# Kernel optimization log

Measured on AMD Instinct MI355X. Metric: run time of the kernel, lower is better.

The kernel has to match this reference:

```python
import jax, jax.numpy as jnp
import numpy as np

FEAT_STRIDE = 8
IM_DIMS = (4096.0, 4096.0)  # (height, width)
ANCHOR_SCALES = (8.0, 16.0, 32.0)
RATIOS = (0.5, 1.0, 2.0)
PRE_NMS_TOPN = 12000   # TRAIN cfg (eval_mode=False)
POST_NMS_TOPN = 2000
NMS_THRESH = 0.7
MIN_SIZE = 16.0


def _generate_anchors(base_size=16.0, ratios=RATIOS, scales=ANCHOR_SCALES):
    ratios = np.array(ratios, np.float32)
    scales = np.array(scales, np.float32)
    w = h = float(base_size)
    x_ctr = 0.5 * (w - 1.0)
    y_ctr = 0.5 * (h - 1.0)
    size = w * h
    ws = np.round(np.sqrt(size / ratios))
    hs = np.round(ws * ratios)
    out = []
    for wr, hr in zip(ws, hs):
        wss = wr * scales
        hss = hr * scales
        out.append(np.stack([x_ctr - 0.5 * (wss - 1.0), y_ctr - 0.5 * (hss - 1.0),
                             x_ctr + 0.5 * (wss - 1.0), y_ctr + 0.5 * (hss - 1.0)], axis=1))
    return np.concatenate(out, 0).astype(np.float32)  # [A=9, 4]


def _nms(boxes, scores, thresh, max_out):
    # greedy sequential NMS; indices are discrete -> stop gradients here
    boxes = jax.lax.stop_gradient(boxes)
    scores = jax.lax.stop_gradient(scores)
    areas = (boxes[:, 2] - boxes[:, 0] + 1.0) * (boxes[:, 3] - boxes[:, 1] + 1.0)

    def body(i, state):
        supp, keep = state
        idx = jnp.argmax(jnp.where(supp, -jnp.inf, scores))
        b = boxes[idx]
        xx1 = jnp.maximum(b[0], boxes[:, 0])
        yy1 = jnp.maximum(b[1], boxes[:, 1])
        xx2 = jnp.minimum(b[2], boxes[:, 2])
        yy2 = jnp.minimum(b[3], boxes[:, 3])
        inter = jnp.maximum(0.0, xx2 - xx1 + 1.0) * jnp.maximum(0.0, yy2 - yy1 + 1.0)
        iou = inter / (areas[idx] + areas - inter)
        supp = supp | (iou > thresh)  # also suppresses idx itself (iou==1)
        keep = keep.at[i].set(idx.astype(jnp.int32))
        return supp, keep

    supp0 = jnp.zeros(boxes.shape[0], dtype=bool)
    keep0 = jnp.zeros(max_out, dtype=jnp.int32)
    _, keep = jax.lax.fori_loop(0, max_out, body, (supp0, keep0))
    return keep


def reference(rpn_cls_score, rpn_bbox_pred):
    _, H, W, C2 = rpn_cls_score.shape
    A = C2 // 2
    # rpn_softmax: per-anchor 2-way (bg, fg) softmax; channels laid out [2, A]
    prob = jax.nn.softmax(rpn_cls_score.reshape(H, W, 2, A), axis=2)
    scores = prob[:, :, 1, :].reshape(-1)           # fg scores, [H*W*A]
    deltas = rpn_bbox_pred.reshape(-1, 4)           # [H*W*A, 4]

    # anchors shifted over the feature grid
    anchors = jnp.asarray(_generate_anchors())       # [A, 4]
    sx = jnp.arange(W, dtype=jnp.float32) * FEAT_STRIDE
    sy = jnp.arange(H, dtype=jnp.float32) * FEAT_STRIDE
    shift_x, shift_y = jnp.meshgrid(sx, sy)          # [H, W]
    shifts = jnp.stack([shift_x, shift_y, shift_x, shift_y], -1).reshape(-1, 1, 4)
    all_anchors = (anchors[None, :, :] + shifts).reshape(-1, 4)  # [H*W*A, 4]

    # bbox_transform_inv
    ws = all_anchors[:, 2] - all_anchors[:, 0] + 1.0
    hs = all_anchors[:, 3] - all_anchors[:, 1] + 1.0
    cx = all_anchors[:, 0] + 0.5 * ws
    cy = all_anchors[:, 1] + 0.5 * hs
    dx, dy, dw, dh = deltas[:, 0], deltas[:, 1], deltas[:, 2], deltas[:, 3]
    pcx = dx * ws + cx
    pcy = dy * hs + cy
    pw = jnp.exp(dw) * ws
    ph = jnp.exp(dh) * hs
    x1 = pcx - 0.5 * pw
    y1 = pcy - 0.5 * ph
    x2 = pcx + 0.5 * pw
    y2 = pcy + 0.5 * ph

    # clip to image boundaries
    x1 = jnp.clip(x1, 0.0, IM_DIMS[1] - 1.0)
    y1 = jnp.clip(y1, 0.0, IM_DIMS[0] - 1.0)
    x2 = jnp.clip(x2, 0.0, IM_DIMS[1] - 1.0)
    y2 = jnp.clip(y2, 0.0, IM_DIMS[0] - 1.0)
    proposals = jnp.stack([x1, y1, x2, y2], axis=1)

    # drop tiny boxes (jit-friendly: -inf score instead of physical removal)
    keep_min = ((x2 - x1 + 1.0) >= MIN_SIZE) & ((y2 - y1 + 1.0) >= MIN_SIZE)
    scores = jnp.where(keep_min, scores, -jnp.inf)

    top_scores, order = jax.lax.top_k(scores, PRE_NMS_TOPN)
    props = proposals[order]                         # [pre_nms_topN, 4]
    keep = _nms(props, top_scores, NMS_THRESH, POST_NMS_TOPN)
    rois = props[keep]                               # [post_nms_topN, 4]
    # blob: [batch_idx(=0), x1, y1, x2, y2]
    return jnp.concatenate([jnp.zeros((POST_NMS_TOPN, 1), rois.dtype), rois], axis=1)


def setup_inputs() -> dict:
    key = jax.random.key(0)
    k1, k2 = jax.random.split(key)
    rpn_cls_score = jax.random.normal(k1, (1, 512, 512, 18), dtype=jnp.float32)
    rpn_bbox_pred = jax.random.normal(k2, (1, 512, 512, 36), dtype=jnp.float32) * 0.2
    return {"rpn_cls_score": rpn_cls_score, "rpn_bbox_pred": rpn_bbox_pred}
```

## Files before the change

kernel.cpp:

```cpp
#include <hip/hip_runtime.h>
#include <cstdint>
#include <cstddef>

#pragma clang fp contract(off)

#define N_ANCH 2359296
#define K_PRE  12000
#define K_POST 2000
#define NWORD  188
#define NC     94
#define TIE_CAP 65536

typedef unsigned int u32;
typedef unsigned long long u64;

__constant__ float c_anch[9][4] = {
  { -84.f,  -40.f,   99.f,   55.f },
  { -176.f, -88.f,  191.f,  103.f },
  { -360.f, -184.f, 375.f,  199.f },
  { -56.f,  -56.f,   71.f,   71.f },
  { -120.f, -120.f, 135.f,  135.f },
  { -248.f, -248.f, 263.f,  263.f },
  { -36.f,  -80.f,   51.f,   95.f },
  { -80.f,  -168.f,  95.f,  183.f },
  { -168.f, -344.f, 183.f,  359.f },
};

__device__ __forceinline__ float pexpf(float xin) {
#pragma clang fp contract(off)
  const float exp_hi = 88.3762626647950f;
  const float exp_lo = -88.3762626647949f;
  const float LOG2EF = 1.44269504088896341f;
  const float C1 = 0.693359375f;
  const float C2 = -2.12194440e-4f;
  const float p0 = 1.9875691500E-4f;
  const float p1 = 1.3981999507E-3f;
  const float p2 = 8.3334519073E-3f;
  const float p3 = 4.1665795894E-2f;
  const float p4 = 1.6666665459E-1f;
  const float p5 = 5.0000001201E-1f;
  float x = fminf(fmaxf(xin, exp_lo), exp_hi);
  float fx = floorf(x * LOG2EF + 0.5f);
  float tmp = C1 * fx;
  float z = C2 * fx;
  x = x - tmp;
  x = x - z;
  z = x * x;
  float y = x * p0 + p1;
  y = y * x + p2;
  y = y * x + p3;
  y = y * x + p4;
  y = y * x + p5;
  y = y * z + x;
  y = 1.0f + y;
  int n = (int)fx;
  u32 e = ((u32)(n + 127)) << 23;
  return y * __uint_as_float(e);
}

__device__ __forceinline__ void decode_box(const float* __restrict__ bbox, int aidx,
                                           float4* ob, float* oarea, bool* okeep) {
#pragma clang fp contract(off)
  int pos = aidx / 9;
  int a = aidx - pos * 9;
  int w = pos & 511;
  int h = pos >> 9;
  float shx = (float)(w * 8);
  float shy = (float)(h * 8);
  float ax1 = c_anch[a][0] + shx;
  float ay1 = c_anch[a][1] + shy;
  float ax2 = c_anch[a][2] + shx;
  float ay2 = c_anch[a][3] + shy;
  float aw = (ax2 - ax1) + 1.0f;
  float ah = (ay2 - ay1) + 1.0f;
  float acx = ax1 + 0.5f * aw;
  float acy = ay1 + 0.5f * ah;
  const float* d = bbox + (size_t)pos * 36 + (size_t)a * 4;
  float dx = d[0], dy = d[1], dw = d[2], dh = d[3];
  float pcx = dx * aw + acx;
  float pcy = dy * ah + acy;
  float pw = pexpf(dw) * aw;
  float ph = pexpf(dh) * ah;
  float x1 = pcx - 0.5f * pw;
  float y1 = pcy - 0.5f * ph;
  float x2 = pcx + 0.5f * pw;
  float y2 = pcy + 0.5f * ph;
  x1 = fminf(fmaxf(x1, 0.0f), 4095.0f);
  y1 = fminf(fmaxf(y1, 0.0f), 4095.0f);
  x2 = fminf(fmaxf(x2, 0.0f), 4095.0f);
  y2 = fminf(fmaxf(y2, 0.0f), 4095.0f);
  *ob = make_float4(x1, y1, x2, y2);
  float ww = (x2 - x1) + 1.0f;
  float hh = (y2 - y1) + 1.0f;
  *oarea = ww * hh;
  *okeep = (ww >= 16.0f) && (hh >= 16.0f);
}

__global__ void k_scores(const float* __restrict__ cls, const float* __restrict__ bbox,
                         u32* __restrict__ keys, u32* __restrict__ ctl,
                         u32* __restrict__ hist) {
#pragma clang fp contract(off)
  int t = blockIdx.x * blockDim.x + threadIdx.x;
  if (blockIdx.x == 0) {
    if (threadIdx.x < 16) ctl[threadIdx.x] = (threadIdx.x == 1) ? (u32)K_PRE : 0u;
    if (threadIdx.x < 256) hist[threadIdx.x] = 0u;
  }
  if (t >= N_ANCH) return;
  int pos = t / 9;
  int a = t - pos * 9;
  float s0 = cls[(size_t)pos * 18 + a];
  float s1 = cls[(size_t)pos * 18 + 9 + a];
  float m = fmaxf(s0, s1);
  float e0 = pexpf(s0 - m);
  float e1 = pexpf(s1 - m);
  float p = e1 / (e0 + e1);
  float4 box; float area; bool km;
  decode_box(bbox, t, &box, &area, &km);
  keys[t] = km ? (__float_as_uint(p) | 0x80000000u) : 0u;
}

__global__ void __launch_bounds__(1024) k_histscan(const u32* __restrict__ keys,
                                                   u32* __restrict__ ctl,
                                                   u32* __restrict__ hist,
                                                   int shift, int pass) {
  __shared__ u32 lh[4][256];
  __shared__ u32 s_last;
  int t = threadIdx.x;
  if (t < 256) { lh[0][t] = 0u; lh[1][t] = 0u; lh[2][t] = 0u; lh[3][t] = 0u; }
  __syncthreads();
  int sub = t & 3;
  u32 prefix = ctl[0];
  u32 msk = (shift == 24) ? 0u : (0xFFFFFFFFu << (shift + 8));
  int stride = gridDim.x * blockDim.x;
  for (int i = blockIdx.x * blockDim.x + t; i < N_ANCH; i += stride) {
    u32 k = keys[i];
    if ((k & msk) == prefix) atomicAdd(&lh[sub][(k >> shift) & 0xFFu], 1u);
  }
  __syncthreads();
  if (t < 256) {
    u32 hsum = lh[0][t] + lh[1][t] + lh[2][t] + lh[3][t];
    if (hsum) atomicAdd(&hist[t], hsum);
  }
  __syncthreads();
  if (t == 0) {
    __threadfence();
    u32 old = atomicAdd(&ctl[8 + pass], 1u);
    s_last = (old == gridDim.x - 1) ? 1u : 0u;
  }
  __syncthreads();
  if (!s_last) return;
  __threadfence();
  __shared__ u32 sh[256];
  __shared__ u32 horig[256];
  __shared__ int s_d;
  u32 h = 0;
  if (t < 256) {
    h = atomicAdd(&hist[t], 0u);
    sh[t] = h; horig[t] = h;
  }
  if (t == 0) s_d = 0;
  u32 krem = ctl[1];
  __syncthreads();
  u32 v = h;
  for (int off = 1; off < 256; off <<= 1) {
    u32 add = (t < 256 && t + off < 256) ? sh[t + off] : 0u;
    __syncthreads();
    if (t < 256) { v += add; sh[t] = v; }
    __syncthreads();
  }
  if (t < 256 && sh[t] >= krem) atomicMax(&s_d, t);
  __syncthreads();
  if (t == 0) {
    int d = s_d;
    u32 cum = sh[d] - horig[d];
    ctl[0] |= ((u32)d) << shift;
    ctl[1] = krem - cum;
    if (shift == 0) { ctl[2] = ctl[0]; ctl[3] = ctl[1]; }
  }
  if (t < 256) hist[t] = 0u;
}

__global__ void __launch_bounds__(1024) k_collect(const u32* __restrict__ keys,
                                                  u32* __restrict__ ctl,
                                                  int* __restrict__ sel,
                                                  int* __restrict__ tie,
                                                  u64* __restrict__ comps) {
  __shared__ int stI[2048];
  __shared__ u64 stC[2048];
  __shared__ int stT[256];
  __shared__ u32 s_cnt, s_tcnt, s_base, s_tbase;
  int tid = threadIdx.x;
  if (tid == 0) { s_cnt = 0; s_tcnt = 0; }
  __syncthreads();
  u32 kstar = ctl[2];
  int stride = gridDim.x * blockDim.x;
  for (int i = blockIdx.x * blockDim.x + tid; i < N_ANCH; i += stride) {
    u32 k = keys[i];
    if (k > kstar) {
      u32 p = atomicAdd(&s_cnt, 1u);
      u64 cmp = ((u64)k << 32) | (u64)(0xFFFFFFFFu - (u32)i);
      if (p < 2048u) { stI[p] = i; stC[p] = cmp; }
      else { u32 g = atomicAdd(&ctl[4], 1u); sel[g] = i; comps[g] = cmp; }
    } else if (k == kstar) {
      u32 p = atomicAdd(&s_tcnt, 1u);
      if (p < 256u) stT[p] = i;
      else { u32 g = atomicAdd(&ctl[5], 1u); if (g < TIE_CAP) tie[g] = i; }
    }
  }
  __syncthreads();
  if (tid == 0) {
    u32 n = min(s_cnt, 2048u);
    s_base = atomicAdd(&ctl[4], n);
    u32 tn = min(s_tcnt, 256u);
    s_tbase = atomicAdd(&ctl[5], tn);
  }
  __syncthreads();
  u32 n = min(s_cnt, 2048u);
  for (u32 q = tid; q < n; q += blockDim.x) {
    sel[s_base + q] = stI[q];
    comps[s_base + q] = stC[q];
  }
  u32 tn = min(s_tcnt, 256u);
  for (u32 q = tid; q < tn; q += blockDim.x) {
    u32 g = s_tbase + q;
    if (g < TIE_CAP) tie[g] = stT[q];
  }
}

__global__ void k_tiepick(const u32* __restrict__ ctl, const int* __restrict__ tie,
                          int* __restrict__ sel, u64* __restrict__ comps) {
  u32 T = ctl[5]; if (T > TIE_CAP) T = TIE_CAP;
  if (T > 8192u) T = 8192u;
  u32 need = ctl[3];
  u32 base = ctl[4];
  u32 kstar = ctl[2];
  for (u32 t = threadIdx.x; t < T; t += blockDim.x) {
    int v = tie[t];
    u32 r = 0;
    for (u32 u = 0; u < T; ++u) r += (tie[u] < v) ? 1u : 0u;
    if (r < need) {
      sel[base + r] = v;
      comps[base + r] = ((u64)kstar << 32) | (u64)(0xFFFFFFFFu - (u32)v);
    }
  }
}

__global__ void k_rankdec(const u64* __restrict__ comps, const int* __restrict__ sel,
                          const float* __restrict__ bbox,
                          float4* __restrict__ props, float* __restrict__ areas) {
  __shared__ u64 tile[2048];
  int tid = threadIdx.x;
  int lane = tid & 63;
  int wave = tid >> 6;
  int base = (blockIdx.x * 4 + wave) * 8;
  u64 c0 = comps[base + 0], c1 = comps[base + 1], c2 = comps[base + 2], c3 = comps[base + 3];
  u64 c4 = comps[base + 4], c5 = comps[base + 5], c6 = comps[base + 6], c7 = comps[base + 7];
  int n0 = 0, n1 = 0, n2 = 0, n3 = 0, n4 = 0, n5 = 0, n6 = 0, n7 = 0;
  for (int t0 = 0; t0 < K_PRE; t0 += 2048) {
    int cnt = min(2048, K_PRE - t0);
    __syncthreads();
    for (int q = tid; q < cnt; q += 256) tile[q] = comps[t0 + q];
    __syncthreads();
    for (int q = lane; q < cnt; q += 64) {
      u64 v = tile[q];
      n0 += (v > c0); n1 += (v > c1); n2 += (v > c2); n3 += (v > c3);
      n4 += (v > c4); n5 += (v > c5); n6 += (v > c6); n7 += (v > c7);
    }
  }
  for (int off = 32; off; off >>= 1) {
    n0 += __shfl_xor(n0, off); n1 += __shfl_xor(n1, off);
    n2 += __shfl_xor(n2, off); n3 += __shfl_xor(n3, off);
    n4 += __shfl_xor(n4, off); n5 += __shfl_xor(n5, off);
    n6 += __shfl_xor(n6, off); n7 += __shfl_xor(n7, off);
  }
  int rk = n0;
  rk = (lane == 1) ? n1 : rk; rk = (lane == 2) ? n2 : rk;
  rk = (lane == 3) ? n3 : rk; rk = (lane == 4) ? n4 : rk;
  rk = (lane == 5) ? n5 : rk; rk = (lane == 6) ? n6 : rk;
  rk = (lane == 7) ? n7 : rk;
  if (lane < 8) {
    float4 box; float area; bool km;
    decode_box(bbox, sel[base + lane], &box, &area, &km);
    props[rk] = box;
    areas[rk] = area;
  }
}

__device__ __forceinline__ int d2idx(int c, int h, int lane) {
  return ((c * 2 + h) * 64 + lane) * 2;
}

__global__ void k_mask(const float4* __restrict__ props, const float* __restrict__ areas,
                       u64* __restrict__ mask, u64* __restrict__ diag2,
                       u64* __restrict__ sub2) {
#pragma clang fp contract(off)
  int x = blockIdx.x, y = blockIdx.y;
  int cx = x >> 1, cy = y >> 1;
  if (cy + 1 < cx || cy == cx + 1) return;
  __shared__ float4 bj[64];
  __shared__ float aj[64];
  int j0 = y * 64;
  bj[threadIdx.x] = props[j0 + threadIdx.x];
  aj[threadIdx.x] = areas[j0 + threadIdx.x];
  __syncthreads();
  int i = x * 64 + threadIdx.x;
  float4 bi = props[i];
  float ai = areas[i];
  u64 bits = 0;
  for (int jj = 0; jj < 64; ++jj) {
    int j = j0 + jj;
    float4 bb = bj[jj];
    float xx1 = fmaxf(bi.x, bb.x);
    float yy1 = fmaxf(bi.y, bb.y);
    float xx2 = fminf(bi.z, bb.z);
    float yy2 = fminf(bi.w, bb.w);
    float w = fmaxf(0.0f, (xx2 - xx1) + 1.0f);
    float h = fmaxf(0.0f, (yy2 - yy1) + 1.0f);
    float inter = w * h;
    float iou = inter / ((ai + aj[jj]) - inter);
    if ((iou > 0.7f) && (j < K_PRE)) bits |= (1ull << jj);
  }
  if (cy == cx)          diag2[d2idx(cx, x & 1, threadIdx.x) + (y & 1)] = bits;
  else if (cy == cx - 1) sub2[d2idx(cx, x & 1, threadIdx.x) + (y & 1)] = bits;
  else                   mask[(size_t)i * NWORD + y] = bits;
}

#define NMS_BAR() asm volatile("s_waitcnt lgkmcnt(0)\n\ts_barrier" ::: "memory")

typedef __attribute__((address_space(1))) const u32* gas_p;
typedef __attribute__((address_space(3))) u32* las_p;
__device__ __forceinline__ void gll16(const u64* g, u64* l) {
  __builtin_amdgcn_global_load_lds((gas_p)g, (las_p)l, 16, 0, 0);
}

__global__ void __launch_bounds__(1024, 1) k_nms(const u64* __restrict__ mask,
                                                 const u64* __restrict__ diag2,
                                                 const u64* __restrict__ sub2,
                                                 const float4* __restrict__ props,
                                                 float* __restrict__ out) {
  __shared__ u64 rem[NWORD];
  __shared__ int keepb[K_POST];
  __shared__ int kept[2][128];
  __shared__ u64 dstage[2][2][64][2];
  __shared__ u64 sstage[2][2][64][2];
  __shared__ int s_kk[2];
  __shared__ int s_nk;
  __shared__ int s_brk;
  int tid = threadIdx.x;
  int lane = tid & 63;
  int wave = tid >> 6;
  for (int w = tid; w < NWORD; w += 1024) {
    int base = w * 64;
    u64 v;
    if (base + 64 <= K_PRE) v = 0ull;
    else if (base >= K_PRE) v = ~0ull;
    else v = (~0ull) << (K_PRE - base);
    rem[w] = v;
  }
  if (tid == 0) { s_nk = 0; s_brk = 0; s_kk[0] = 0; s_kk[1] = 0; }
  if (wave == 0) {
    gll16(diag2 + d2idx(0, 0, lane), &dstage[0][0][0][0]);
    gll16(diag2 + d2idx(0, 1, lane), &dstage[0][1][0][0]);
    gll16(sub2 + d2idx(1, 0, lane), &sstage[1][0][0][0]);
    gll16(sub2 + d2idx(1, 1, lane), &sstage[1][1][0][0]);
  }
  __syncthreads();

  int nk = 0;

  for (int c = 0; c < NC; ++c) {
    if (s_brk) break;
    int par = c & 1;
    if (wave == 0) {
      int cn = min(c + 1, NC - 1);
      int cs = min(c + 2, NC - 1);
      gll16(diag2 + d2idx(cn, 0, lane), &dstage[cn & 1][0][0][0]);
      gll16(diag2 + d2idx(cn, 1, lane), &dstage[cn & 1][1][0][0]);
      gll16(sub2 + d2idx(cs, 0, lane), &sstage[cs & 1][0][0][0]);
      gll16(sub2 + d2idx(cs, 1, lane), &sstage[cs & 1][1][0][0]);
      asm volatile("s_waitcnt vmcnt(4)" ::: "memory");
      u64 dl0A = dstage[par][0][lane][0], dl1A = dstage[par][0][lane][1];
      u64 dh0A = dstage[par][1][lane][0], dh1A = dstage[par][1][lane][1];
      int ps = (c + 1) & 1;
      u64 sl0A = sstage[ps][0][lane][0], sl1A = sstage[ps][0][lane][1];
      u64 sh0A = sstage[ps][1][lane][0], sh1A = sstage[ps][1][lane][1];
      u64 w0 = ~rem[2 * c];
      u64 w1 = ~rem[2 * c + 1];
      u64 km0 = 0, km1 = 0;
      int nk0 = nk;
      while (w0 != 0ull && nk < K_POST) {
        int j = (int)__builtin_ctzll(w0);
        u64 sup = __ballot((int)((dl0A >> j) & 1ull));
        km0 |= (1ull << j);
        nk++;
        w0 &= ~sup;
      }
      if (km0) w1 &= ~__ballot((int)((dh0A & km0) != 0ull));
      while (w1 != 0ull && nk < K_POST) {
        int j = (int)__builtin_ctzll(w1);
        u64 sup = __ballot((int)((dh1A >> j) & 1ull));
        km1 |= (1ull << j);
        nk++;
        w1 &= ~sup;
      }
      int ncnt0 = __popcll(km0);
      u64 below = (1ull << lane) - 1ull;
      if ((km0 >> lane) & 1ull) {
        int pos = nk0 + __popcll(km0 & below);
        int idx = (c << 7) | lane;
        keepb[pos] = idx;
        kept[par][pos - nk0] = idx;
      }
      if ((km1 >> lane) & 1ull) {
        int pos = nk0 + ncnt0 + __popcll(km1 & below);
        int idx = (c << 7) | 64 | lane;
        keepb[pos] = idx;
        kept[par][pos - nk0] = idx;
      }
      if (c + 1 < NC) {
        int plo = (int)((((sl0A & km0) | (sl1A & km1)) != 0ull) ? 1 : 0);
        int phi = (int)((((sh0A & km0) | (sh1A & km1)) != 0ull) ? 1 : 0);
        u64 vlo = __ballot(plo);
        u64 vhi = __ballot(phi);
        if (lane == 0) {
          if (vlo) atomicOr((unsigned long long*)&rem[2 * c + 2], (unsigned long long)vlo);
          if (vhi) atomicOr((unsigned long long*)&rem[2 * c + 3], (unsigned long long)vhi);
        }
      }
      if (lane == 0) { s_kk[par] = nk - nk0; s_nk = nk; s_brk = (nk >= K_POST) ? 1 : 0; }
    } else if (c >= 1) {
      int kkp = s_kk[par ^ 1];
      const int* kb = &kept[par ^ 1][0];
      int wv = wave - 1;
      int seg = wv % 3;
      int q0 = wv / 3;
      int w = 2 * c + 2 + seg * 64 + lane;
      if (kkp > q0 && w < NWORD) {
        int m = kkp - 1;
        const u64* p0 = mask + (size_t)kb[q0] * NWORD + w;
        const u64* p1 = mask + (size_t)kb[min(q0 + 5, m)] * NWORD + w;
        const u64* p2 = mask + (size_t)kb[min(q0 + 10, m)] * NWORD + w;
        const u64* p3 = mask + (size_t)kb[min(q0 + 15, m)] * NWORD + w;
        const u64* p4 = mask + (size_t)kb[min(q0 + 20, m)] * NWORD + w;
        const u64* p5 = mask + (size_t)kb[min(q0 + 25, m)] * NWORD + w;
        const u64* p6 = mask + (size_t)kb[min(q0 + 30, m)] * NWORD + w;
        const u64* p7 = mask + (size_t)kb[min(q0 + 35, m)] * NWORD + w;
        u64 fp0, fp1, fp2, fp3, fp4, fp5, fp6, fp7;
        asm volatile(
          "global_load_dwordx2 %0, %8, off\n\t"
          "global_load_dwordx2 %1, %9, off\n\t"
          "global_load_dwordx2 %2, %10, off\n\t"
          "global_load_dwordx2 %3, %11, off\n\t"
          "global_load_dwordx2 %4, %12, off\n\t"
          "global_load_dwordx2 %5, %13, off\n\t"
          "global_load_dwordx2 %6, %14, off\n\t"
          "global_load_dwordx2 %7, %15, off\n\t"
          "s_waitcnt vmcnt(0)"
          : "=&v"(fp0), "=&v"(fp1), "=&v"(fp2), "=&v"(fp3),
            "=&v"(fp4), "=&v"(fp5), "=&v"(fp6), "=&v"(fp7)
          : "v"(p0), "v"(p1), "v"(p2), "v"(p3),
            "v"(p4), "v"(p5), "v"(p6), "v"(p7)
          : "memory");
        u64 v = (fp0 | fp1) | (fp2 | fp3) | ((fp4 | fp5) | (fp6 | fp7));
        for (int q = q0 + 40; q < kkp; q += 5)
          v |= mask[(size_t)kb[q] * NWORD + w];
        if (v) atomicOr((unsigned long long*)&rem[w], (unsigned long long)v);
      }
    }
    NMS_BAR();
  }
  __syncthreads();
  int fnk = s_nk;
  for (int t = tid; t < K_POST; t += 1024) {
    int kidx = (t < fnk) ? keepb[t] : 0;
    float4 b = props[kidx];
    out[t * 5 + 0] = 0.0f;
    out[t * 5 + 1] = b.x;
    out[t * 5 + 2] = b.y;
    out[t * 5 + 3] = b.z;
    out[t * 5 + 4] = b.w;
  }
}

extern "C" void kernel_launch(void* const* d_in, const int* in_sizes, int n_in,
                              void* d_out, int out_size, void* d_ws, size_t ws_size,
                              hipStream_t stream) {
  const float* cls  = (const float*)d_in[0];
  const float* bbox = (const float*)d_in[1];
  float* out = (float*)d_out;
  char* ws = (char*)d_ws;

  u64* mask    = (u64*)ws;
  u32* keys    = (u32*)ws;
  u32* ctl     = (u32*)(ws + 9437184);
  u32* hist    = (u32*)(ws + 9437248);
  int* sel     = (int*)(ws + 9438464);
  int* tie     = (int*)(ws + 9486592);
  u64* comps   = (u64*)(ws + 18096128);
  float4* props= (float4*)(ws + 18240512);
  float* areas = (float*)(ws + 18433024);
  u64* diag2   = (u64*)(ws + 18481152);
  u64* sub2    = (u64*)(ws + 18673664);

  k_scores<<<dim3((N_ANCH + 255) / 256), dim3(256), 0, stream>>>(cls, bbox, keys, ctl, hist);
  const int shifts[4] = {24, 16, 8, 0};
  for (int s = 0; s < 4; ++s)
    k_histscan<<<dim3(256), dim3(1024), 0, stream>>>(keys, ctl, hist, shifts[s], s);
  k_collect<<<dim3(256), dim3(1024), 0, stream>>>(keys, ctl, sel, tie, comps);
  k_tiepick<<<dim3(1), dim3(256), 0, stream>>>(ctl, tie, sel, comps);
  k_rankdec<<<dim3(375), dim3(256), 0, stream>>>(comps, sel, bbox, props, areas);
  k_mask<<<dim3(188, 188), dim3(64), 0, stream>>>(props, areas, mask, diag2, sub2);
  k_nms<<<dim3(1), dim3(1024), 0, stream>>>(mask, diag2, sub2, props, out);
}
```

Before: 304.8 us.

## Widen NMS chunks to 256 boxes to halve block barriers

```diff
diff --git a/kernel.cpp b/kernel.cpp
--- a/kernel.cpp
+++ b/kernel.cpp
@@ -8,7 +8,7 @@
 #define K_PRE  12000
 #define K_POST 2000
 #define NWORD  188
-#define NC     94
+#define NC     47
 #define TIE_CAP 65536
 
 typedef unsigned int u32;
@@ -286,17 +286,18 @@
   }
 }
 
-__device__ __forceinline__ int d2idx(int c, int h, int lane) {
-  return ((c * 2 + h) * 64 + lane) * 2;
+__device__ __forceinline__ size_t d4off(int c, int g, int h) {
+  return ((size_t)((c * 4 + g) * 2 + h)) * 128;
 }
 
 __global__ void k_mask(const float4* __restrict__ props, const float* __restrict__ areas,
-                       u64* __restrict__ mask, u64* __restrict__ diag2,
-                       u64* __restrict__ sub2) {
+                       u64* __restrict__ mask, u64* __restrict__ diag4,
+                       u64* __restrict__ sub4) {
 #pragma clang fp contract(off)
   int x = blockIdx.x, y = blockIdx.y;
-  int cx = x >> 1, cy = y >> 1;
-  if (cy + 1 < cx || cy == cx + 1) return;
+  int cx = x >> 2, cy = y >> 2;
+  bool wd = (cy == cx), ws = (cy == cx - 1), wf = (cy >= cx + 2);
+  if (!(wd || ws || wf)) return;
   __shared__ float4 bj[64];
   __shared__ float aj[64];
   int j0 = y * 64;
@@ -320,9 +321,16 @@
     float iou = inter / ((ai + aj[jj]) - inter);
     if ((iou > 0.7f) && (j < K_PRE)) bits |= (1ull << jj);
   }
-  if (cy == cx)          diag2[d2idx(cx, x & 1, threadIdx.x) + (y & 1)] = bits;
-  else if (cy == cx - 1) sub2[d2idx(cx, x & 1, threadIdx.x) + (y & 1)] = bits;
-  else                   mask[(size_t)i * NWORD + y] = bits;
+  int g = x & 3;
+  if (wd) {
+    int wi = y - 4 * cx;
+    diag4[d4off(cx, g, wi >> 1) + 2 * threadIdx.x + (wi & 1)] = bits;
+  } else if (ws) {
+    int wi = y - 4 * (cx - 1);
+    sub4[d4off(cx, g, wi >> 1) + 2 * threadIdx.x + (wi & 1)] = bits;
+  } else {
+    mask[(size_t)i * NWORD + y] = bits;
+  }
 }
 
 #define NMS_BAR() asm volatile("s_waitcnt lgkmcnt(0)\n\ts_barrier" ::: "memory")
@@ -334,15 +342,15 @@
 }
 
 __global__ void __launch_bounds__(1024, 1) k_nms(const u64* __restrict__ mask,
-                                                 const u64* __restrict__ diag2,
-                                                 const u64* __restrict__ sub2,
+                                                 const u64* __restrict__ diag4,
+                                                 const u64* __restrict__ sub4,
                                                  const float4* __restrict__ props,
                                                  float* __restrict__ out) {
   __shared__ u64 rem[NWORD];
   __shared__ int keepb[K_POST];
-  __shared__ int kept[2][128];
-  __shared__ u64 dstage[2][2][64][2];
-  __shared__ u64 sstage[2][2][64][2];
+  __shared__ int kept[2][256];
+  __shared__ u64 dstage[2][4][2][64][2];
+  __shared__ u64 sstage[2][4][2][64][2];
   __shared__ int s_kk[2];
   __shared__ int s_nk;
   __shared__ int s_brk;
@@ -359,10 +367,13 @@
   }
   if (tid == 0) { s_nk = 0; s_brk = 0; s_kk[0] = 0; s_kk[1] = 0; }
   if (wave == 0) {
-    gll16(diag2 + d2idx(0, 0, lane), &dstage[0][0][0][0]);
-    gll16(diag2 + d2idx(0, 1, lane), &dstage[0][1][0][0]);
-    gll16(sub2 + d2idx(1, 0, lane), &sstage[1][0][0][0]);
-    gll16(sub2 + d2idx(1, 1, lane), &sstage[1][1][0][0]);
+#pragma unroll
+    for (int g = 0; g < 4; ++g) {
+      gll16(diag4 + d4off(0, g, 0) + 2 * lane, &dstage[0][g][0][0][0]);
+      gll16(diag4 + d4off(0, g, 1) + 2 * lane, &dstage[0][g][1][0][0]);
+      gll16(sub4 + d4off(1, g, 0) + 2 * lane, &sstage[1][g][0][0][0]);
+      gll16(sub4 + d4off(1, g, 1) + 2 * lane, &sstage[1][g][1][0][0]);
+    }
   }
   __syncthreads();
 
@@ -374,57 +385,119 @@
     if (wave == 0) {
       int cn = min(c + 1, NC - 1);
       int cs = min(c + 2, NC - 1);
-      gll16(diag2 + d2idx(cn, 0, lane), &dstage[cn & 1][0][0][0]);
-      gll16(diag2 + d2idx(cn, 1, lane), &dstage[cn & 1][1][0][0]);
-      gll16(sub2 + d2idx(cs, 0, lane), &sstage[cs & 1][0][0][0]);
-      gll16(sub2 + d2idx(cs, 1, lane), &sstage[cs & 1][1][0][0]);
-      asm volatile("s_waitcnt vmcnt(4)" ::: "memory");
-      u64 dl0A = dstage[par][0][lane][0], dl1A = dstage[par][0][lane][1];
-      u64 dh0A = dstage[par][1][lane][0], dh1A = dstage[par][1][lane][1];
-      int ps = (c + 1) & 1;
-      u64 sl0A = sstage[ps][0][lane][0], sl1A = sstage[ps][0][lane][1];
-      u64 sh0A = sstage[ps][1][lane][0], sh1A = sstage[ps][1][lane][1];
-      u64 w0 = ~rem[2 * c];
-      u64 w1 = ~rem[2 * c + 1];
-      u64 km0 = 0, km1 = 0;
+#pragma unroll
+      for (int g = 0; g < 4; ++g) {
+        gll16(diag4 + d4off(cn, g, 0) + 2 * lane, &dstage[cn & 1][g][0][0][0]);
+        gll16(diag4 + d4off(cn, g, 1) + 2 * lane, &dstage[cn & 1][g][1][0][0]);
+        gll16(sub4 + d4off(cs, g, 0) + 2 * lane, &sstage[cs & 1][g][0][0][0]);
+        gll16(sub4 + d4off(cs, g, 1) + 2 * lane, &sstage[cs & 1][g][1][0][0]);
+      }
+      asm volatile("s_waitcnt vmcnt(16)" ::: "memory");
+      u64 w0 = ~rem[4 * c];
+      u64 w1 = ~rem[4 * c + 1];
+      u64 w2 = ~rem[4 * c + 2];
+      u64 w3 = ~rem[4 * c + 3];
+      u64 km0 = 0, km1 = 0, km2 = 0, km3 = 0;
       int nk0 = nk;
-      while (w0 != 0ull && nk < K_POST) {
-        int j = (int)__builtin_ctzll(w0);
-        u64 sup = __ballot((int)((dl0A >> j) & 1ull));
-        km0 |= (1ull << j);
-        nk++;
-        w0 &= ~sup;
-      }
-      if (km0) w1 &= ~__ballot((int)((dh0A & km0) != 0ull));
-      while (w1 != 0ull && nk < K_POST) {
-        int j = (int)__builtin_ctzll(w1);
-        u64 sup = __ballot((int)((dh1A >> j) & 1ull));
-        km1 |= (1ull << j);
-        nk++;
-        w1 &= ~sup;
-      }
-      int ncnt0 = __popcll(km0);
+      {
+        u64 d00 = dstage[par][0][0][lane][0];
+        while (w0 != 0ull && nk < K_POST) {
+          int j = (int)__builtin_ctzll(w0);
+          u64 sup = __ballot((int)((d00 >> j) & 1ull));
+          km0 |= (1ull << j);
+          nk++;
+          w0 &= ~sup;
+        }
+        if (km0) {
+          u64 d10 = dstage[par][1][0][lane][0];
+          u64 d20 = dstage[par][2][0][lane][0];
+          u64 d30 = dstage[par][3][0][lane][0];
+          w1 &= ~__ballot((int)((d10 & km0) != 0ull));
+          w2 &= ~__ballot((int)((d20 & km0) != 0ull));
+          w3 &= ~__ballot((int)((d30 & km0) != 0ull));
+        }
+      }
+      {
+        u64 d11 = dstage[par][1][0][lane][1];
+        while (w1 != 0ull && nk < K_POST) {
+          int j = (int)__builtin_ctzll(w1);
+          u64 sup = __ballot((int)((d11 >> j) & 1ull));
+          km1 |= (1ull << j);
+          nk++;
+          w1 &= ~sup;
+        }
+        if (km1) {
+          u64 d21 = dstage[par][2][0][lane][1];
+          u64 d31 = dstage[par][3][0][lane][1];
+          w2 &= ~__ballot((int)((d21 & km1) != 0ull));
+          w3 &= ~__ballot((int)((d31 & km1) != 0ull));
+        }
+      }
+      {
+        u64 d22 = dstage[par][2][1][lane][0];
+        while (w2 != 0ull && nk < K_POST) {
+          int j = (int)__builtin_ctzll(w2);
+          u64 sup = __ballot((int)((d22 >> j) & 1ull));
+          km2 |= (1ull << j);
+          nk++;
+          w2 &= ~sup;
+        }
+        if (km2) {
+          u64 d32 = dstage[par][3][1][lane][0];
+          w3 &= ~__ballot((int)((d32 & km2) != 0ull));
+        }
+      }
+      {
+        u64 d33 = dstage[par][3][1][lane][1];
+        while (w3 != 0ull && nk < K_POST) {
+          int j = (int)__builtin_ctzll(w3);
+          u64 sup = __ballot((int)((d33 >> j) & 1ull));
+          km3 |= (1ull << j);
+          nk++;
+          w3 &= ~sup;
+        }
+      }
+      int p0 = __popcll(km0), p1 = __popcll(km1), p2 = __popcll(km2);
       u64 below = (1ull << lane) - 1ull;
       if ((km0 >> lane) & 1ull) {
         int pos = nk0 + __popcll(km0 & below);
-        int idx = (c << 7) | lane;
-        keepb[pos] = idx;
-        kept[par][pos - nk0] = idx;
+        int idx = (c << 8) | lane;
+        keepb[pos] = idx; kept[par][pos - nk0] = idx;
       }
       if ((km1 >> lane) & 1ull) {
-        int pos = nk0 + ncnt0 + __popcll(km1 & below);
-        int idx = (c << 7) | 64 | lane;
-        keepb[pos] = idx;
-        kept[par][pos - nk0] = idx;
+        int pos = nk0 + p0 + __popcll(km1 & below);
+        int idx = (c << 8) | 64 | lane;
+        keepb[pos] = idx; kept[par][pos - nk0] = idx;
+      }
+      if ((km2 >> lane) & 1ull) {
+        int pos = nk0 + p0 + p1 + __popcll(km2 & below);
+        int idx = (c << 8) | 128 | lane;
+        keepb[pos] = idx; kept[par][pos - nk0] = idx;
+      }
+      if ((km3 >> lane) & 1ull) {
+        int pos = nk0 + p0 + p1 + p2 + __popcll(km3 & below);
+        int idx = (c << 8) | 192 | lane;
+        keepb[pos] = idx; kept[par][pos - nk0] = idx;
       }
       if (c + 1 < NC) {
-        int plo = (int)((((sl0A & km0) | (sl1A & km1)) != 0ull) ? 1 : 0);
-        int phi = (int)((((sh0A & km0) | (sh1A & km1)) != 0ull) ? 1 : 0);
-        u64 vlo = __ballot(plo);
-        u64 vhi = __ballot(phi);
+        int ps = (c + 1) & 1;
+        u64 a0 = (sstage[ps][0][0][lane][0] & km0) | (sstage[ps][0][0][lane][1] & km1)
+               | (sstage[ps][0][1][lane][0] & km2) | (sstage[ps][0][1][lane][1] & km3);
+        u64 a1 = (sstage[ps][1][0][lane][0] & km0) | (sstage[ps][1][0][lane][1] & km1)
+               | (sstage[ps][1][1][lane][0] & km2) | (sstage[ps][1][1][lane][1] & km3);
+        u64 a2 = (sstage[ps][2][0][lane][0] & km0) | (sstage[ps][2][0][lane][1] & km1)
+               | (sstage[ps][2][1][lane][0] & km2) | (sstage[ps][2][1][lane][1] & km3);
+        u64 a3 = (sstage[ps][3][0][lane][0] & km0) | (sstage[ps][3][0][lane][1] & km1)
+               | (sstage[ps][3][1][lane][0] & km2) | (sstage[ps][3][1][lane][1] & km3);
+        u64 v0 = __ballot((int)(a0 != 0ull));
+        u64 v1 = __ballot((int)(a1 != 0ull));
+        u64 v2 = __ballot((int)(a2 != 0ull));
+        u64 v3 = __ballot((int)(a3 != 0ull));
         if (lane == 0) {
-          if (vlo) atomicOr((unsigned long long*)&rem[2 * c + 2], (unsigned long long)vlo);
-          if (vhi) atomicOr((unsigned long long*)&rem[2 * c + 3], (unsigned long long)vhi);
+          if (v0) atomicOr((unsigned long long*)&rem[4 * c + 4], (unsigned long long)v0);
+          if (v1) atomicOr((unsigned long long*)&rem[4 * c + 5], (unsigned long long)v1);
+          if (v2) atomicOr((unsigned long long*)&rem[4 * c + 6], (unsigned long long)v2);
+          if (v3) atomicOr((unsigned long long*)&rem[4 * c + 7], (unsigned long long)v3);
         }
       }
       if (lane == 0) { s_kk[par] = nk - nk0; s_nk = nk; s_brk = (nk >= K_POST) ? 1 : 0; }
@@ -434,35 +507,39 @@
       int wv = wave - 1;
       int seg = wv % 3;
       int q0 = wv / 3;
-      int w = 2 * c + 2 + seg * 64 + lane;
+      int w = 4 * c + 4 + seg * 64 + lane;
       if (kkp > q0 && w < NWORD) {
         int m = kkp - 1;
-        const u64* p0 = mask + (size_t)kb[q0] * NWORD + w;
-        const u64* p1 = mask + (size_t)kb[min(q0 + 5, m)] * NWORD + w;
-        const u64* p2 = mask + (size_t)kb[min(q0 + 10, m)] * NWORD + w;
-        const u64* p3 = mask + (size_t)kb[min(q0 + 15, m)] * NWORD + w;
-        const u64* p4 = mask + (size_t)kb[min(q0 + 20, m)] * NWORD + w;
-        const u64* p5 = mask + (size_t)kb[min(q0 + 25, m)] * NWORD + w;
-        const u64* p6 = mask + (size_t)kb[min(q0 + 30, m)] * NWORD + w;
-        const u64* p7 = mask + (size_t)kb[min(q0 + 35, m)] * NWORD + w;
-        u64 fp0, fp1, fp2, fp3, fp4, fp5, fp6, fp7;
+        const u64* a0 = mask + (size_t)kb[q0] * NWORD + w;
+        const u64* a1 = mask + (size_t)kb[min(q0 + 5, m)] * NWORD + w;
+        const u64* a2 = mask + (size_t)kb[min(q0 + 10, m)] * NWORD + w;
+        const u64* a3 = mask + (size_t)kb[min(q0 + 15, m)] * NWORD + w;
+        const u64* a4 = mask + (size_t)kb[min(q0 + 20, m)] * NWORD + w;
+        const u64* a5 = mask + (size_t)kb[min(q0 + 25, m)] * NWORD + w;
+        const u64* a6 = mask + (size_t)kb[min(q0 + 30, m)] * NWORD + w;
+        const u64* a7 = mask + (size_t)kb[min(q0 + 35, m)] * NWORD + w;
+        const u64* a8 = mask + (size_t)kb[min(q0 + 40, m)] * NWORD + w;
+        const u64* a9 = mask + (size_t)kb[min(q0 + 45, m)] * NWORD + w;
+        u64 f0, f1, f2, f3, f4, f5, f6, f7, f8, f9;
         asm volatile(
-          "global_load_dwordx2 %0, %8, off\n\t"
-          "global_load_dwordx2 %1, %9, off\n\t"
-          "global_load_dwordx2 %2, %10, off\n\t"
-          "global_load_dwordx2 %3, %11, off\n\t"
-          "global_load_dwordx2 %4, %12, off\n\t"
-          "global_load_dwordx2 %5, %13, off\n\t"
-          "global_load_dwordx2 %6, %14, off\n\t"
-          "global_load_dwordx2 %7, %15, off\n\t"
+          "global_load_dwordx2 %0, %10, off\n\t"
+          "global_load_dwordx2 %1, %11, off\n\t"
+          "global_load_dwordx2 %2, %12, off\n\t"
+          "global_load_dwordx2 %3, %13, off\n\t"
+          "global_load_dwordx2 %4, %14, off\n\t"
+          "global_load_dwordx2 %5, %15, off\n\t"
+          "global_load_dwordx2 %6, %16, off\n\t"
+          "global_load_dwordx2 %7, %17, off\n\t"
+          "global_load_dwordx2 %8, %18, off\n\t"
+          "global_load_dwordx2 %9, %19, off\n\t"
           "s_waitcnt vmcnt(0)"
-          : "=&v"(fp0), "=&v"(fp1), "=&v"(fp2), "=&v"(fp3),
-            "=&v"(fp4), "=&v"(fp5), "=&v"(fp6), "=&v"(fp7)
-          : "v"(p0), "v"(p1), "v"(p2), "v"(p3),
-            "v"(p4), "v"(p5), "v"(p6), "v"(p7)
+          : "=&v"(f0), "=&v"(f1), "=&v"(f2), "=&v"(f3), "=&v"(f4),
+            "=&v"(f5), "=&v"(f6), "=&v"(f7), "=&v"(f8), "=&v"(f9)
+          : "v"(a0), "v"(a1), "v"(a2), "v"(a3), "v"(a4),
+            "v"(a5), "v"(a6), "v"(a7), "v"(a8), "v"(a9)
           : "memory");
-        u64 v = (fp0 | fp1) | (fp2 | fp3) | ((fp4 | fp5) | (fp6 | fp7));
-        for (int q = q0 + 40; q < kkp; q += 5)
+        u64 v = ((f0 | f1) | (f2 | f3)) | ((f4 | f5) | (f6 | f7)) | (f8 | f9);
+        for (int q = q0 + 50; q < kkp; q += 5)
           v |= mask[(size_t)kb[q] * NWORD + w];
         if (v) atomicOr((unsigned long long*)&rem[w], (unsigned long long)v);
       }
@@ -499,8 +576,8 @@
   u64* comps   = (u64*)(ws + 18096128);
   float4* props= (float4*)(ws + 18240512);
   float* areas = (float*)(ws + 18433024);
-  u64* diag2   = (u64*)(ws + 18481152);
-  u64* sub2    = (u64*)(ws + 18673664);
+  u64* diag4   = (u64*)(ws + 18481152);
+  u64* sub4    = (u64*)(ws + 18866176);
 
   k_scores<<<dim3((N_ANCH + 255) / 256), dim3(256), 0, stream>>>(cls, bbox, keys, ctl, hist);
   const int shifts[4] = {24, 16, 8, 0};
@@ -509,6 +586,6 @@
   k_collect<<<dim3(256), dim3(1024), 0, stream>>>(keys, ctl, sel, tie, comps);
   k_tiepick<<<dim3(1), dim3(256), 0, stream>>>(ctl, tie, sel, comps);
   k_rankdec<<<dim3(375), dim3(256), 0, stream>>>(comps, sel, bbox, props, areas);
-  k_mask<<<dim3(188, 188), dim3(64), 0, stream>>>(props, areas, mask, diag2, sub2);
-  k_nms<<<dim3(1), dim3(1024), 0, stream>>>(mask, diag2, sub2, props, out);
-}
+  k_mask<<<dim3(188, 188), dim3(64), 0, stream>>>(props, areas, mask, diag4, sub4);
+  k_nms<<<dim3(1), dim3(1024), 0, stream>>>(mask, diag4, sub4, props, out);
+}
```

Result: slower. 310.9 us (+2.0%).
